# Performance work log

Hardware: AMD Instinct MI355X
Metric: run time of the kernel (lower is better)

Reference implementation:

```python
import jax, jax.numpy as jnp
import numpy as np
from jax import lax


def T_grid(t, num_coeff):
    # Chebyshev polynomials T_0..T_{N-1} evaluated at t -> (N, len(t))
    rows = [jnp.ones_like(t), t]
    for _ in range(2, num_coeff):
        rows.append(2.0 * t * rows[-1] - rows[-2])
    return jnp.stack(rows[:num_coeff], axis=0)


def setup_inputs() -> dict:
    key = jax.random.key(0)
    k1, k2, k3, k4, k5 = jax.random.split(key, 5)
    B, D, H, N, T = 128, 512, 1024, 32, 16
    return {
        "t_span": jnp.linspace(0.0, 1.0, T, dtype=jnp.float32),
        "y_init": jax.random.normal(k1, (B, D), dtype=jnp.float32),
        "B_init": jax.random.uniform(k2, (B, D, N), dtype=jnp.float32),
        "W1": jax.random.normal(k3, (D, H), dtype=jnp.float32) / jnp.sqrt(jnp.float32(D)),
        "b1": jax.random.normal(k4, (H,), dtype=jnp.float32),
        "W2": jax.random.normal(k5, (H, D), dtype=jnp.float32) / jnp.sqrt(jnp.float32(H)),
        "num_coeff_per_dim": 32,
        "max_iters": 10,
    }


def reference(t_span, y_init, B_init, W1, b1, W2, num_coeff_per_dim, max_iters):
    N = num_coeff_per_dim
    t0, t1 = t_span[0], t_span[-1]

    # Chebyshev-Gauss-Lobatto nodes on [-1, 1] and Simpson midpoints interleaved
    t_cheb = -jnp.cos(jnp.pi * (jnp.arange(N, dtype=t_span.dtype) / (N - 1)))  # (N,)
    mids = 0.5 * (t_cheb[1:] + t_cheb[:-1])
    t_simpsons = jnp.zeros(2 * N - 1, dtype=t_span.dtype).at[::2].set(t_cheb).at[1::2].set(mids)
    t_true = t0 + 0.5 * (t1 - t0) * (t_simpsons + 1.0)  # (2N-1,)

    Phi_f = T_grid(t_simpsons, N)        # (N, 2N-1)
    Phi = Phi_f[:, ::2]                  # (N, N), invert ONCE (reused every iter)
    Phi_inv = jnp.linalg.inv(Phi)
    widths = (t_true[2::2] - t_true[:-2:2]) / 6.0  # (N-1,) Simpson interval weights

    def f_all(Y):  # vector field f(t, y) = tanh(y @ W1 + t*b1) @ W2, all nodes at once
        # Y: (B, D, M) with M = 2N-1
        h = jnp.tanh(jnp.einsum("bdm,dh->bhm", Y, W1) + t_true[None, None, :] * b1[None, :, None])
        return jnp.einsum("bhm,hd->bdm", h, W2)

    def step(Bc, _):
        approx = jnp.einsum("bdn,nm->bdm", Bc, Phi_f)          # (B, D, 2N-1)
        fap = f_all(approx)
        # Simpson's rule per Chebyshev interval, then cumulative integral S
        s = widths * (fap[..., :-2:2] + 4.0 * fap[..., 1:-1:2] + fap[..., 2::2])  # (B,D,N-1)
        S = jnp.concatenate([jnp.zeros_like(s[..., :1]), jnp.cumsum(s, axis=-1)], axis=-1)
        # torch.linalg.solve(Phi, S + y0, left=False): Bn @ Phi = S + y0
        Bn = (S + y_init[..., None]) @ Phi_inv
        return Bn, None

    B_final, _ = lax.scan(step, B_init, None, length=max_iters)

    t_out = -1.0 + 2.0 * (t_span - t0) / (t1 - t0)
    Phi_out = T_grid(t_out, N)                                  # (N, T)
    approx = jnp.einsum("bdn,nt->bdt", B_final, Phi_out)        # (B, D, T)
    return jnp.moveaxis(approx, -1, 0), B_final                 # (T, B, D), (B, D, N)
```

## Files before the change

kernel.cpp:

```cpp
#include <hip/hip_runtime.h>
#include <hip/hip_bf16.h>
#include <math.h>

#define BB 128
#define DD 512
#define HH 1024
#define NB 32
#define MM 63
#define TT 16
#define ITERS 10

#define OFF_U       0
#define OFF_TTRUE   64
#define OFF_PHIOUT  128
#define OFF_PHIF_BF 1024
#define OFF_QT_BF   2048
#define HDRF        4096
#define OFF_PTPA    HDRF
#define OFF_PTP0    (OFF_PTPA + 2097152)
#define OFF_W1P     (OFF_PTP0 + 2097152)
#define OFF_W2P     (OFF_W1P + 262144)
#define OFF_WWP     (OFF_W2P + 262144)
#define OFF_YW1     (OFF_WWP + 524288)

typedef __attribute__((ext_vector_type(8))) short bf16x8;
typedef __attribute__((ext_vector_type(4))) float f32x4;

static __device__ __forceinline__ unsigned short f2bf(float f) {
    unsigned int x = __builtin_bit_cast(unsigned int, f);
    unsigned int r = x + 0x7FFFu + ((x >> 16) & 1u);
    return (unsigned short)(r >> 16);
}

static __device__ __forceinline__ void store4bf(unsigned short* p,
                                                float v0, float v1, float v2, float v3) {
    unsigned int lo = (unsigned int)f2bf(v0) | ((unsigned int)f2bf(v1) << 16);
    unsigned int hi = (unsigned int)f2bf(v2) | ((unsigned int)f2bf(v3) << 16);
    uint2 u; u.x = lo; u.y = hi;
    *(uint2*)p = u;
}

static __device__ __forceinline__ float tanh_fast(float x) {
    float e = exp2f(x * 2.88539008177793f);
    return 1.0f - 2.0f / (e + 1.0f);
}

static __device__ __forceinline__ unsigned short* aS(unsigned short* smA, int r, int c16) {
    return (unsigned short*)((char*)smA + (((r << 10) + (c16 << 4)) ^ ((r & 7) << 4)));
}

__global__ __launch_bounds__(256) void prologue_kernel(
        const float* __restrict__ t_span, const float* __restrict__ W1,
        const float* __restrict__ W2, const float* __restrict__ y_init,
        float* __restrict__ ws) {
    __shared__ __align__(16) char smem[66560];
    const int bid  = blockIdx.x;
    const int t    = threadIdx.x;
    const int lane = t & 63;
    const int w    = t >> 6;
    const int q    = lane >> 4;
    const int l15  = lane & 15;

    if (bid == 0) {
        double* tsim    = (double*)(smem + 0);
        double* ttrue_d = (double*)(smem + 512);
        double* wid     = (double*)(smem + 1024);
        double* phid    = (double*)(smem + 1280);
        double* aug     = (double*)(smem + 17408);
        double* mlt     = (double*)(smem + 33792);
        double* Rl      = (double*)(smem + 34048);
        double* Qd      = (double*)(smem + 50176);
        int*    piv_s   = (int*)(smem + 66304);

        const int rgrp = t >> 6;
        const double PI = 3.14159265358979323846;
        const double t0 = (double)t_span[0];
        const double t1 = (double)t_span[TT - 1];

        if (t < MM) {
            double v;
            if ((t & 1) == 0) {
                int j = t >> 1;
                v = -cos(PI * (double)j / (double)(NB - 1));
            } else {
                int i = t >> 1;
                double a = -cos(PI * (double)i / (double)(NB - 1));
                double b = -cos(PI * (double)(i + 1) / (double)(NB - 1));
                v = 0.5 * (a + b);
            }
            tsim[t] = v;
            ttrue_d[t] = t0 + 0.5 * (t1 - t0) * (v + 1.0);
        }
        __syncthreads();
        if (t < 31) wid[t] = (ttrue_d[2 * t + 2] - ttrue_d[2 * t]) / 6.0;
        if (t < MM) ws[OFF_TTRUE + t] = (float)ttrue_d[t];
        if (t == 63) ws[OFF_TTRUE + 63] = 0.0f;

        if (t < MM) {
            double x = tsim[t];
            double r0 = 1.0, r1 = x;
            phid[0 * MM + t] = r0;
            phid[1 * MM + t] = r1;
            for (int n = 2; n < NB; n++) {
                double r2 = 2.0 * x * r1 - r0;
                phid[n * MM + t] = r2;
                r0 = r1; r1 = r2;
            }
        }
        __syncthreads();

        {
            unsigned short* pf = (unsigned short*)(ws + OFF_PHIF_BF);
            for (int f = t; f < 64 * 32; f += 256) {
                int m = f >> 5, n = f & 31;
                pf[f] = f2bf(m < MM ? (float)phid[n * MM + m] : 0.0f);
            }
        }

        for (int f = t; f < NB * 64; f += 256) {
            int r = f >> 6, c = f & 63;
            double v;
            if (c < NB) v = phid[r * MM + 2 * c];
            else        v = ((c - NB) == r) ? 1.0 : 0.0;
            aug[f] = v;
        }
        __syncthreads();

        for (int k = 0; k < NB; k++) {
            if (t < 32) {
                double v = (t >= k) ? fabs(aug[t * 64 + k]) : -1.0;
                int idx = t;
                #pragma unroll
                for (int off = 16; off >= 1; off >>= 1) {
                    double ov = __shfl_xor(v, off);
                    int    oi = __shfl_xor(idx, off);
                    if (ov > v) { v = ov; idx = oi; }
                }
                if (t == 0) *piv_s = idx;
            }
            __syncthreads();
            const int p = *piv_s;
            if (t < 64) {
                double pv   = aug[p * 64 + k];
                double rowp = aug[p * 64 + t];
                double rowk = aug[k * 64 + t];
                aug[k * 64 + t] = rowp / pv;
                if (p != k) aug[p * 64 + t] = rowk;
            }
            __syncthreads();
            if (t < 32) mlt[t] = (t == k) ? 0.0 : aug[t * 64 + k];
            __syncthreads();
            {
                double pk = aug[k * 64 + lane];
                #pragma unroll
                for (int i = 0; i < 8; i++) {
                    int r = rgrp * 8 + i;
                    aug[r * 64 + lane] -= mlt[r] * pk;
                }
            }
            __syncthreads();
        }

        if (t < MM) {
            double acc = 0.0;
            Rl[t * NB + 0] = 0.0;
            for (int i = 1; i < NB; i++) {
                int ip = i - 1;
                double wv = 0.0;
                if (t == 2 * ip)     wv += wid[ip];
                if (t == 2 * ip + 1) wv += 4.0 * wid[ip];
                if (t == 2 * ip + 2) wv += wid[ip];
                acc += wv;
                Rl[t * NB + i] = acc;
            }
        }
        __syncthreads();

        for (int f = t; f < MM * NB; f += 256) {
            int m = f >> 5, j = f & 31;
            double s = 0.0;
            for (int i = 0; i < NB; i++) s += Rl[m * NB + i] * aug[i * 64 + 32 + j];
            Qd[f] = s;
        }
        __syncthreads();

        {
            unsigned short* qt = (unsigned short*)(ws + OFF_QT_BF);
            for (int f = t; f < 32 * 64; f += 256) {
                int j = f >> 6, m = f & 63;
                qt[f] = f2bf(m < MM ? (float)Qd[m * NB + j] : 0.0f);
            }
        }
        if (t < NB) {
            double s = 0.0;
            for (int i = 0; i < NB; i++) s += aug[i * 64 + 32 + t];
            ws[OFF_U + t] = (float)s;
        }
        if (t < TT) {
            double x = -1.0 + 2.0 * ((double)t_span[t] - t0) / (t1 - t0);
            double r0 = 1.0, r1 = x;
            ws[OFF_PHIOUT + 0 * TT + t] = 1.0f;
            ws[OFF_PHIOUT + 1 * TT + t] = (float)x;
            for (int n = 2; n < NB; n++) {
                double r2 = 2.0 * x * r1 - r0;
                ws[OFF_PHIOUT + n * TT + t] = (float)r2;
                r0 = r1; r1 = r2;
            }
        }
        return;
    }

    if (bid <= 64) {
        unsigned short* W1p = (unsigned short*)(ws + OFF_W1P);
        const int hb = bid - 1;
        #pragma unroll
        for (int i = 0; i < 4; i++) {
            int f = i * 256 + t;
            int ds = f >> 6, ln = f & 63;
            int qq = ln >> 4, ll = ln & 15;
            unsigned short tmp[8];
            #pragma unroll
            for (int e = 0; e < 8; e++)
                tmp[e] = f2bf(W1[(size_t)(ds * 32 + qq * 8 + e) * HH + hb * 16 + ll]);
            *(uint4*)(W1p + ((size_t)(hb * 16 + ds) * 64 + ln) * 8) = *(uint4*)tmp;
        }
        return;
    }

    if (bid <= 96) {
        unsigned short* W2p = (unsigned short*)(ws + OFF_W2P);
        const int db = bid - 65;
        #pragma unroll
        for (int i = 0; i < 8; i++) {
            int f = i * 256 + t;
            int hs = f >> 6, ln = f & 63;
            int qq = ln >> 4, ll = ln & 15;
            unsigned short tmp[8];
            #pragma unroll
            for (int e = 0; e < 8; e++)
                tmp[e] = f2bf(W2[(size_t)(hs * 32 + qq * 8 + e) * DD + db * 16 + ll]);
            *(uint4*)(W2p + ((size_t)(db * 32 + hs) * 64 + ln) * 8) = *(uint4*)tmp;
        }
        return;
    }

    unsigned short* lw1 = (unsigned short*)smem;

    if (bid <= 352) {
        unsigned short* WWp = (unsigned short*)(ws + OFF_WWP);
        unsigned short* pbounce = (unsigned short*)(smem + 36864);
        const int idx   = bid - 97;
        const int h2grp = idx & 31;
        const int hpb   = (idx >> 5) * 4 + w;
        const int h2c0  = h2grp * 32;

        for (int i = 0; i < 64; i++) {
            int f = i * 256 + t;
            int row = f >> 5, col = f & 31;
            lw1[row * 36 + col] = f2bf(W1[(size_t)row * HH + h2c0 + col]);
        }
        __syncthreads();

        f32x4 acc[2][2] = {};
        #pragma unroll 4
        for (int ds = 0; ds < 16; ds++) {
            bf16x8 a[2];
            #pragma unroll
            for (int mt = 0; mt < 2; mt++) {
                const float* w2r = W2 + (size_t)(hpb * 32 + mt * 16 + l15) * DD + ds * 32 + q * 8;
                float4 va = *(const float4*)w2r;
                float4 vb = *(const float4*)(w2r + 4);
                unsigned short tmp[8] = { f2bf(va.x), f2bf(va.y), f2bf(va.z), f2bf(va.w),
                                          f2bf(vb.x), f2bf(vb.y), f2bf(vb.z), f2bf(vb.w) };
                a[mt] = *(bf16x8*)tmp;
            }
            bf16x8 bb0, bb1;
            {
                unsigned short tb[8];
                #pragma unroll
                for (int e = 0; e < 8; e++)
                    tb[e] = lw1[(ds * 32 + q * 8 + e) * 36 + l15];
                bb0 = *(bf16x8*)tb;
                #pragma unroll
                for (int e = 0; e < 8; e++)
                    tb[e] = lw1[(ds * 32 + q * 8 + e) * 36 + 16 + l15];
                bb1 = *(bf16x8*)tb;
            }
            acc[0][0] = __builtin_amdgcn_mfma_f32_16x16x32_bf16(a[0], bb0, acc[0][0], 0, 0, 0);
            acc[0][1] = __builtin_amdgcn_mfma_f32_16x16x32_bf16(a[0], bb1, acc[0][1], 0, 0, 0);
            acc[1][0] = __builtin_amdgcn_mfma_f32_16x16x32_bf16(a[1], bb0, acc[1][0], 0, 0, 0);
            acc[1][1] = __builtin_amdgcn_mfma_f32_16x16x32_bf16(a[1], bb1, acc[1][1], 0, 0, 0);
        }
        unsigned short* pb = pbounce + w * 1024;
        #pragma unroll
        for (int mt = 0; mt < 2; mt++)
            #pragma unroll
            for (int nt = 0; nt < 2; nt++) {
                int lane8 = (mt * 2 + (q >> 1)) * 16 + l15;
                #pragma unroll
                for (int r = 0; r < 4; r++)
                    pb[(nt * 64 + lane8) * 8 + (q & 1) * 4 + r] = f2bf(acc[mt][nt][r]);
            }
        uint4 f0 = *(uint4*)(pb + (0 * 64 + lane) * 8);
        uint4 f1 = *(uint4*)(pb + (1 * 64 + lane) * 8);
        int h2b0 = h2grp * 2;
        *(uint4*)(WWp + ((size_t)(h2b0 + 0) * 32 + hpb) * 512 + lane * 8) = f0;
        *(uint4*)(WWp + ((size_t)(h2b0 + 1) * 32 + hpb) * 512 + lane * 8) = f1;
        return;
    }

    {
        float* yW1 = ws + OFF_YW1;
        const int h2grp = bid - 353;
        const int h2c0  = h2grp * 32;

        for (int i = 0; i < 64; i++) {
            int f = i * 256 + t;
            int row = f >> 5, col = f & 31;
            lw1[row * 36 + col] = f2bf(W1[(size_t)row * HH + h2c0 + col]);
        }
        __syncthreads();

        f32x4 acc[2][2] = {};
        #pragma unroll 4
        for (int ds = 0; ds < 16; ds++) {
            bf16x8 a[2];
            #pragma unroll
            for (int mt = 0; mt < 2; mt++) {
                const float* yr = y_init + (size_t)(w * 32 + mt * 16 + l15) * DD + ds * 32 + q * 8;
                float4 va = *(const float4*)yr;
                float4 vb = *(const float4*)(yr + 4);
                unsigned short tmp[8] = { f2bf(va.x), f2bf(va.y), f2bf(va.z), f2bf(va.w),
                                          f2bf(vb.x), f2bf(vb.y), f2bf(vb.z), f2bf(vb.w) };
                a[mt] = *(bf16x8*)tmp;
            }
            bf16x8 bb0, bb1;
            {
                unsigned short tb[8];
                #pragma unroll
                for (int e = 0; e < 8; e++)
                    tb[e] = lw1[(ds * 32 + q * 8 + e) * 36 + l15];
                bb0 = *(bf16x8*)tb;
                #pragma unroll
                for (int e = 0; e < 8; e++)
                    tb[e] = lw1[(ds * 32 + q * 8 + e) * 36 + 16 + l15];
                bb1 = *(bf16x8*)tb;
            }
            acc[0][0] = __builtin_amdgcn_mfma_f32_16x16x32_bf16(a[0], bb0, acc[0][0], 0, 0, 0);
            acc[0][1] = __builtin_amdgcn_mfma_f32_16x16x32_bf16(a[0], bb1, acc[0][1], 0, 0, 0);
            acc[1][0] = __builtin_amdgcn_mfma_f32_16x16x32_bf16(a[1], bb0, acc[1][0], 0, 0, 0);
            acc[1][1] = __builtin_amdgcn_mfma_f32_16x16x32_bf16(a[1], bb1, acc[1][1], 0, 0, 0);
        }
        #pragma unroll
        for (int mt = 0; mt < 2; mt++)
            #pragma unroll
            for (int nt = 0; nt < 2; nt++)
                #pragma unroll
                for (int r = 0; r < 4; r++) {
                    int b  = w * 32 + mt * 16 + q * 4 + r;
                    int h2 = h2c0 + nt * 16 + l15;
                    yW1[(size_t)b * HH + h2] = acc[mt][nt][r];
                }
    }
}

__global__ __launch_bounds__(256) void k1_kernel(
        const float* __restrict__ B_init,
        const unsigned short* __restrict__ W1p,
        const float* __restrict__ b1,
        const float* __restrict__ ws,
        unsigned short* __restrict__ Ptp)
{
    __shared__ __align__(16) char smem[40960];
    unsigned short* smA  = (unsigned short*)smem;
    unsigned short* t_sb = (unsigned short*)smem;
    unsigned short* g_sb = (unsigned short*)(smem + 32768);

    const int t    = threadIdx.x;
    const int lane = t & 63;
    const int w    = t >> 6;
    const int q    = lane >> 4;
    const int l15  = lane & 15;
    const int bid  = blockIdx.x;
    const int b    = bid & 127;
    const int hblk = bid >> 7;
    const int hw   = hblk * 128 + w * 32;

    {
        const float* Bi = B_init + (size_t)b * DD * NB;
        #pragma unroll 8
        for (int i = 0; i < 64; i++) {
            int f = i * 256 + t;
            int d = f >> 5, n = f & 31;
            *(unsigned short*)(smem + (((n << 10) + (d << 1)) ^ ((n & 7) << 4)))
                = f2bf(Bi[f]);
        }
    }
    __syncthreads();

    f32x4 acc[2][2] = {};
    const unsigned short* W1b = W1p + (size_t)(hw >> 4) * 8192;
    #pragma unroll 4
    for (int d0 = 0; d0 < DD; d0 += 32) {
        int c16 = (d0 >> 3) + q;
        int ds  = d0 >> 5;
        bf16x8 a0  = *(const bf16x8*)aS(smA, l15, c16);
        bf16x8 a1  = *(const bf16x8*)aS(smA, 16 + l15, c16);
        bf16x8 bb0 = *(const bf16x8*)(W1b + ds * 512 + lane * 8);
        bf16x8 bb1 = *(const bf16x8*)(W1b + 8192 + ds * 512 + lane * 8);
        acc[0][0] = __builtin_amdgcn_mfma_f32_16x16x32_bf16(a0, bb0, acc[0][0], 0, 0, 0);
        acc[0][1] = __builtin_amdgcn_mfma_f32_16x16x32_bf16(a0, bb1, acc[0][1], 0, 0, 0);
        acc[1][0] = __builtin_amdgcn_mfma_f32_16x16x32_bf16(a1, bb0, acc[1][0], 0, 0, 0);
        acc[1][1] = __builtin_amdgcn_mfma_f32_16x16x32_bf16(a1, bb1, acc[1][1], 0, 0, 0);
    }
    #pragma unroll
    for (int mt = 0; mt < 2; mt++)
        #pragma unroll
        for (int nt = 0; nt < 2; nt++) {
            int hl = w * 32 + nt * 16 + l15;
            store4bf(&g_sb[hl * 32 + mt * 16 + q * 4],
                     acc[mt][nt][0], acc[mt][nt][1], acc[mt][nt][2], acc[mt][nt][3]);
        }
    __syncthreads();

    f32x4 zacc[4][2] = {};
    const unsigned short* PF = (const unsigned short*)(ws + OFF_PHIF_BF);
    bf16x8 gb[2];
    #pragma unroll
    for (int nt = 0; nt < 2; nt++)
        gb[nt] = *(const bf16x8*)(&g_sb[(w * 32 + nt * 16 + l15) * 32 + q * 8]);
    #pragma unroll
    for (int mt = 0; mt < 4; mt++) {
        bf16x8 af = *(const bf16x8*)(PF + (mt * 16 + l15) * 32 + q * 8);
        zacc[mt][0] = __builtin_amdgcn_mfma_f32_16x16x32_bf16(af, gb[0], zacc[mt][0], 0, 0, 0);
        zacc[mt][1] = __builtin_amdgcn_mfma_f32_16x16x32_bf16(af, gb[1], zacc[mt][1], 0, 0, 0);
    }

    const float* TTp = ws + OFF_TTRUE;
    float b1v[2] = { b1[hw + l15], b1[hw + 16 + l15] };
    #pragma unroll
    for (int mt = 0; mt < 4; mt++) {
        float4 ttv = *(const float4*)(TTp + mt * 16 + q * 4);
        #pragma unroll
        for (int nt = 0; nt < 2; nt++) {
            int hl = w * 32 + nt * 16 + l15;
            float v0 = tanh_fast(zacc[mt][nt][0] + ttv.x * b1v[nt]);
            float v1 = tanh_fast(zacc[mt][nt][1] + ttv.y * b1v[nt]);
            float v2 = tanh_fast(zacc[mt][nt][2] + ttv.z * b1v[nt]);
            float v3 = tanh_fast(zacc[mt][nt][3] + ttv.w * b1v[nt]);
            store4bf(&t_sb[hl * 72 + mt * 16 + q * 4], v0, v1, v2, v3);
        }
    }
    __syncthreads();

    f32x4 pacc[2][2] = {};
    const unsigned short* QT = (const unsigned short*)(ws + OFF_QT_BF);
    #pragma unroll
    for (int ks = 0; ks < 2; ks++) {
        bf16x8 bt[2];
        #pragma unroll
        for (int nt = 0; nt < 2; nt++)
            bt[nt] = *(const bf16x8*)(&t_sb[(w * 32 + nt * 16 + l15) * 72 + ks * 32 + q * 8]);
        #pragma unroll
        for (int jt = 0; jt < 2; jt++) {
            bf16x8 aq = *(const bf16x8*)(QT + (jt * 16 + l15) * 64 + ks * 32 + q * 8);
            pacc[jt][0] = __builtin_amdgcn_mfma_f32_16x16x32_bf16(aq, bt[0], pacc[jt][0], 0, 0, 0);
            pacc[jt][1] = __builtin_amdgcn_mfma_f32_16x16x32_bf16(aq, bt[1], pacc[jt][1], 0, 0, 0);
        }
    }

    {
        unsigned short* pb = g_sb + w * 1024;
        #pragma unroll
        for (int jt = 0; jt < 2; jt++)
            #pragma unroll
            for (int nt = 0; nt < 2; nt++) {
                int grp = (nt * 2 + (l15 >> 3)) & 3;
                #pragma unroll
                for (int r = 0; r < 4; r++) {
                    int lane8 = grp * 16 + q * 4 + r;
                    pb[(jt * 64 + lane8) * 8 + (l15 & 7)] = f2bf(pacc[jt][nt][r]);
                }
            }
        int hs = hblk * 4 + w;
        uint4 f0 = *(uint4*)(pb + (0 * 64 + lane) * 8);
        uint4 f1 = *(uint4*)(pb + (1 * 64 + lane) * 8);
        *(uint4*)(Ptp + (((size_t)(b * 32 + hs) * 2 + 0) * 64 + lane) * 8) = f0;
        *(uint4*)(Ptp + (((size_t)(b * 32 + hs) * 2 + 1) * 64 + lane) * 8) = f1;
    }
}

__global__ __launch_bounds__(256) void kf_kernel(
        const unsigned short* __restrict__ Ptin,
        const unsigned short* __restrict__ WWp,
        const float* __restrict__ yW1,
        const float* __restrict__ b1,
        const float* __restrict__ ws,
        unsigned short* __restrict__ Ptout)
{
    __shared__ __align__(16) unsigned short t_sb[128 * 72];
    __shared__ __align__(16) unsigned short g_sb[128 * 32];

    const int t    = threadIdx.x;
    const int lane = t & 63;
    const int w    = t >> 6;
    const int q    = lane >> 4;
    const int l15  = lane & 15;
    const int bid  = blockIdx.x;
    const int b    = bid & 127;
    const int hblk = bid >> 7;
    const int hw   = hblk * 128 + w * 32;

    f32x4 acc[2][2] = {};
    const unsigned short* Ab  = Ptin + (size_t)b * 32768;
    const unsigned short* WWb = WWp + (size_t)(hw >> 4) * 16384;
    #pragma unroll 4
    for (int s = 0; s < 32; s++) {
        bf16x8 a0  = *(const bf16x8*)(Ab + (s * 2 + 0) * 512 + lane * 8);
        bf16x8 a1  = *(const bf16x8*)(Ab + (s * 2 + 1) * 512 + lane * 8);
        bf16x8 bb0 = *(const bf16x8*)(WWb + s * 512 + lane * 8);
        bf16x8 bb1 = *(const bf16x8*)(WWb + 16384 + s * 512 + lane * 8);
        acc[0][0] = __builtin_amdgcn_mfma_f32_16x16x32_bf16(a0, bb0, acc[0][0], 0, 0, 0);
        acc[0][1] = __builtin_amdgcn_mfma_f32_16x16x32_bf16(a0, bb1, acc[0][1], 0, 0, 0);
        acc[1][0] = __builtin_amdgcn_mfma_f32_16x16x32_bf16(a1, bb0, acc[1][0], 0, 0, 0);
        acc[1][1] = __builtin_amdgcn_mfma_f32_16x16x32_bf16(a1, bb1, acc[1][1], 0, 0, 0);
    }

    const float* U = ws + OFF_U;
    float yw[2] = { yW1[(size_t)b * HH + hw + l15],
                    yW1[(size_t)b * HH + hw + 16 + l15] };
    #pragma unroll
    for (int mt = 0; mt < 2; mt++) {
        float4 uv = *(const float4*)(U + mt * 16 + q * 4);
        #pragma unroll
        for (int nt = 0; nt < 2; nt++) {
            int hl = w * 32 + nt * 16 + l15;
            store4bf(&g_sb[hl * 32 + mt * 16 + q * 4],
                     acc[mt][nt][0] + uv.x * yw[nt],
                     acc[mt][nt][1] + uv.y * yw[nt],
                     acc[mt][nt][2] + uv.z * yw[nt],
                     acc[mt][nt][3] + uv.w * yw[nt]);
        }
    }

    f32x4 zacc[4][2] = {};
    const unsigned short* PF = (const unsigned short*)(ws + OFF_PHIF_BF);
    bf16x8 gb[2];
    #pragma unroll
    for (int nt = 0; nt < 2; nt++)
        gb[nt] = *(const bf16x8*)(&g_sb[(w * 32 + nt * 16 + l15) * 32 + q * 8]);
    #pragma unroll
    for (int mt = 0; mt < 4; mt++) {
        bf16x8 af = *(const bf16x8*)(PF + (mt * 16 + l15) * 32 + q * 8);
        zacc[mt][0] = __builtin_amdgcn_mfma_f32_16x16x32_bf16(af, gb[0], zacc[mt][0], 0, 0, 0);
        zacc[mt][1] = __builtin_amdgcn_mfma_f32_16x16x32_bf16(af, gb[1], zacc[mt][1], 0, 0, 0);
    }

    const float* TTp = ws + OFF_TTRUE;
    float b1v[2] = { b1[hw + l15], b1[hw + 16 + l15] };
    #pragma unroll
    for (int mt = 0; mt < 4; mt++) {
        float4 ttv = *(const float4*)(TTp + mt * 16 + q * 4);
        #pragma unroll
        for (int nt = 0; nt < 2; nt++) {
            int hl = w * 32 + nt * 16 + l15;
            float v0 = tanh_fast(zacc[mt][nt][0] + ttv.x * b1v[nt]);
            float v1 = tanh_fast(zacc[mt][nt][1] + ttv.y * b1v[nt]);
            float v2 = tanh_fast(zacc[mt][nt][2] + ttv.z * b1v[nt]);
            float v3 = tanh_fast(zacc[mt][nt][3] + ttv.w * b1v[nt]);
            store4bf(&t_sb[hl * 72 + mt * 16 + q * 4], v0, v1, v2, v3);
        }
    }

    f32x4 pacc[2][2] = {};
    const unsigned short* QT = (const unsigned short*)(ws + OFF_QT_BF);
    #pragma unroll
    for (int ks = 0; ks < 2; ks++) {
        bf16x8 bt[2];
        #pragma unroll
        for (int nt = 0; nt < 2; nt++)
            bt[nt] = *(const bf16x8*)(&t_sb[(w * 32 + nt * 16 + l15) * 72 + ks * 32 + q * 8]);
        #pragma unroll
        for (int jt = 0; jt < 2; jt++) {
            bf16x8 aq = *(const bf16x8*)(QT + (jt * 16 + l15) * 64 + ks * 32 + q * 8);
            pacc[jt][0] = __builtin_amdgcn_mfma_f32_16x16x32_bf16(aq, bt[0], pacc[jt][0], 0, 0, 0);
            pacc[jt][1] = __builtin_amdgcn_mfma_f32_16x16x32_bf16(aq, bt[1], pacc[jt][1], 0, 0, 0);
        }
    }

    {
        unsigned short* pb = g_sb + w * 1024;
        #pragma unroll
        for (int jt = 0; jt < 2; jt++)
            #pragma unroll
            for (int nt = 0; nt < 2; nt++) {
                int grp = (nt * 2 + (l15 >> 3)) & 3;
                #pragma unroll
                for (int r = 0; r < 4; r++) {
                    int lane8 = grp * 16 + q * 4 + r;
                    pb[(jt * 64 + lane8) * 8 + (l15 & 7)] = f2bf(pacc[jt][nt][r]);
                }
            }
        int hs = hblk * 4 + w;
        uint4 f0 = *(uint4*)(pb + (0 * 64 + lane) * 8);
        uint4 f1 = *(uint4*)(pb + (1 * 64 + lane) * 8);
        *(uint4*)(Ptout + (((size_t)(b * 32 + hs) * 2 + 0) * 64 + lane) * 8) = f0;
        *(uint4*)(Ptout + (((size_t)(b * 32 + hs) * 2 + 1) * 64 + lane) * 8) = f1;
    }
}

__global__ __launch_bounds__(256) void k2f_kernel(
        const unsigned short* __restrict__ Ptp,
        const unsigned short* __restrict__ W2p,
        const float* __restrict__ y_init,
        const float* __restrict__ ws,
        float* __restrict__ out)
{
    __shared__ __align__(16) float ls[4 * 544];
    __shared__ float phiout_s[NB * TT];

    const int t    = threadIdx.x;
    const int lane = t & 63;
    const int w    = t >> 6;
    const int q    = lane >> 4;
    const int l15  = lane & 15;
    const int bid  = blockIdx.x;
    const int b    = bid & 127;
    const int dblk = bid >> 7;
    const int dw   = dblk * 64 + w * 16;

    for (int f = t; f < NB * TT; f += 256) phiout_s[f] = ws[OFF_PHIOUT + f];

    f32x4 acc[2] = {};
    const unsigned short* Ab  = Ptp + (size_t)b * 32768;
    const unsigned short* W2b = W2p + (size_t)(dblk * 4 + w) * 16384;
    #pragma unroll 4
    for (int s = 0; s < 32; s++) {
        bf16x8 a0 = *(const bf16x8*)(Ab + (s * 2 + 0) * 512 + lane * 8);
        bf16x8 a1 = *(const bf16x8*)(Ab + (s * 2 + 1) * 512 + lane * 8);
        bf16x8 bb = *(const bf16x8*)(W2b + s * 512 + lane * 8);
        acc[0] = __builtin_amdgcn_mfma_f32_16x16x32_bf16(a0, bb, acc[0], 0, 0, 0);
        acc[1] = __builtin_amdgcn_mfma_f32_16x16x32_bf16(a1, bb, acc[1], 0, 0, 0);
    }

    const float* U = ws + OFF_U;
    float yv = y_init[(size_t)b * DD + dw + l15];
    #pragma unroll
    for (int mt = 0; mt < 2; mt++) {
        float4 uv = *(const float4*)(U + mt * 16 + q * 4);
        #pragma unroll
        for (int r = 0; r < 4; r++) {
            int j = mt * 16 + q * 4 + r;
            float uvr = (r == 0) ? uv.x : (r == 1) ? uv.y : (r == 2) ? uv.z : uv.w;
            ls[w * 544 + j * 17 + l15] = acc[mt][r] + yv * uvr;
        }
    }
    __syncthreads();

    float* out1 = out + (size_t)TT * BB * DD;
    #pragma unroll
    for (int it = 0; it < 8; it++) {
        int f = it * 64 + lane;
        int d_l = f >> 5, j2 = f & 31;
        out1[((size_t)b * DD + dw + d_l) * NB + j2] = ls[w * 544 + j2 * 17 + d_l];
    }

    #pragma unroll
    for (int i = 0; i < 4; i++) {
        int idx = i * 256 + t;
        int t16 = idx >> 6, dl = idx & 63;
        float s = 0.f;
        #pragma unroll
        for (int n = 0; n < NB; n++)
            s += ls[(dl >> 4) * 544 + n * 17 + (dl & 15)] * phiout_s[n * TT + t16];
        out[(size_t)t16 * (BB * DD) + (size_t)b * DD + dblk * 64 + dl] = s;
    }
}

extern "C" void kernel_launch(void* const* d_in, const int* in_sizes, int n_in,
                              void* d_out, int out_size, void* d_ws, size_t ws_size,
                              hipStream_t stream) {
    const float* t_span = (const float*)d_in[0];
    const float* y_init = (const float*)d_in[1];
    const float* B_init = (const float*)d_in[2];
    const float* W1     = (const float*)d_in[3];
    const float* b1     = (const float*)d_in[4];
    const float* W2     = (const float*)d_in[5];
    float* ws  = (float*)d_ws;
    float* out = (float*)d_out;

    unsigned short* W1p  = (unsigned short*)(ws + OFF_W1P);
    unsigned short* W2p  = (unsigned short*)(ws + OFF_W2P);
    unsigned short* WWp  = (unsigned short*)(ws + OFF_WWP);
    float*          yW1  = ws + OFF_YW1;
    unsigned short* PtpA = (unsigned short*)(ws + OFF_PTPA);
    unsigned short* PtpB = (unsigned short*)(ws + OFF_PTP0);

    prologue_kernel<<<dim3(385), 256, 0, stream>>>(t_span, W1, W2, y_init, ws);

    k1_kernel<<<dim3(1024), 256, 0, stream>>>(B_init, W1p, b1, ws, PtpA);

    unsigned short* pin  = PtpA;
    unsigned short* pout = PtpB;
    for (int it = 1; it < ITERS; it++) {
        kf_kernel<<<dim3(1024), 256, 0, stream>>>(pin, WWp, yW1, b1, ws, pout);
        unsigned short* tmp = pin; pin = pout; pout = tmp;
    }
    k2f_kernel<<<dim3(1024), 256, 0, stream>>>(pin, W2p, y_init, ws, out);
}
```

Before: 368.5 us.

## Double the kf tile width, stage A operand in LDS, transpose W1 staging

kf_kernel now gives each wave 64 hidden columns instead of 32 and halves the grid to 512 blocks. The per-batch A operand is double-buffered into shared memory in chunks and each A fragment is reused across four B tiles, which cuts redundant global loads of Ptin. The prologue stores the W1 tile transposed so B fragments are read with one vector LDS load instead of eight scalar loads. The cost is more registers and a 68KB shared buffer per block, which may reduce occupancy and leave fewer blocks to fill the GPU.

```diff
diff --git a/kernel.cpp b/kernel.cpp
--- a/kernel.cpp
+++ b/kernel.cpp
@@ -244,11 +244,11 @@
         return;
     }
 
-    unsigned short* lw1 = (unsigned short*)smem;
+    unsigned short* lw1t = (unsigned short*)smem;
 
     if (bid <= 352) {
         unsigned short* WWp = (unsigned short*)(ws + OFF_WWP);
-        unsigned short* pbounce = (unsigned short*)(smem + 36864);
+        unsigned short* pbounce = (unsigned short*)(smem + 33280);
         const int idx   = bid - 97;
         const int h2grp = idx & 31;
         const int hpb   = (idx >> 5) * 4 + w;
@@ -257,7 +257,7 @@
         for (int i = 0; i < 64; i++) {
             int f = i * 256 + t;
             int row = f >> 5, col = f & 31;
-            lw1[row * 36 + col] = f2bf(W1[(size_t)row * HH + h2c0 + col]);
+            lw1t[col * 520 + row] = f2bf(W1[(size_t)row * HH + h2c0 + col]);
         }
         __syncthreads();
 
@@ -274,18 +274,8 @@
                                           f2bf(vb.x), f2bf(vb.y), f2bf(vb.z), f2bf(vb.w) };
                 a[mt] = *(bf16x8*)tmp;
             }
-            bf16x8 bb0, bb1;
-            {
-                unsigned short tb[8];
-                #pragma unroll
-                for (int e = 0; e < 8; e++)
-                    tb[e] = lw1[(ds * 32 + q * 8 + e) * 36 + l15];
-                bb0 = *(bf16x8*)tb;
-                #pragma unroll
-                for (int e = 0; e < 8; e++)
-                    tb[e] = lw1[(ds * 32 + q * 8 + e) * 36 + 16 + l15];
-                bb1 = *(bf16x8*)tb;
-            }
+            bf16x8 bb0 = *(const bf16x8*)(lw1t + l15 * 520 + ds * 32 + q * 8);
+            bf16x8 bb1 = *(const bf16x8*)(lw1t + (16 + l15) * 520 + ds * 32 + q * 8);
             acc[0][0] = __builtin_amdgcn_mfma_f32_16x16x32_bf16(a[0], bb0, acc[0][0], 0, 0, 0);
             acc[0][1] = __builtin_amdgcn_mfma_f32_16x16x32_bf16(a[0], bb1, acc[0][1], 0, 0, 0);
             acc[1][0] = __builtin_amdgcn_mfma_f32_16x16x32_bf16(a[1], bb0, acc[1][0], 0, 0, 0);
@@ -317,7 +307,7 @@
         for (int i = 0; i < 64; i++) {
             int f = i * 256 + t;
             int row = f >> 5, col = f & 31;
-            lw1[row * 36 + col] = f2bf(W1[(size_t)row * HH + h2c0 + col]);
+            lw1t[col * 520 + row] = f2bf(W1[(size_t)row * HH + h2c0 + col]);
         }
         __syncthreads();
 
@@ -334,18 +324,8 @@
                                           f2bf(vb.x), f2bf(vb.y), f2bf(vb.z), f2bf(vb.w) };
                 a[mt] = *(bf16x8*)tmp;
             }
-            bf16x8 bb0, bb1;
-            {
-                unsigned short tb[8];
-                #pragma unroll
-                for (int e = 0; e < 8; e++)
-                    tb[e] = lw1[(ds * 32 + q * 8 + e) * 36 + l15];
-                bb0 = *(bf16x8*)tb;
-                #pragma unroll
-                for (int e = 0; e < 8; e++)
-                    tb[e] = lw1[(ds * 32 + q * 8 + e) * 36 + 16 + l15];
-                bb1 = *(bf16x8*)tb;
-            }
+            bf16x8 bb0 = *(const bf16x8*)(lw1t + l15 * 520 + ds * 32 + q * 8);
+            bf16x8 bb1 = *(const bf16x8*)(lw1t + (16 + l15) * 520 + ds * 32 + q * 8);
             acc[0][0] = __builtin_amdgcn_mfma_f32_16x16x32_bf16(a[0], bb0, acc[0][0], 0, 0, 0);
             acc[0][1] = __builtin_amdgcn_mfma_f32_16x16x32_bf16(a[0], bb1, acc[0][1], 0, 0, 0);
             acc[1][0] = __builtin_amdgcn_mfma_f32_16x16x32_bf16(a[1], bb0, acc[1][0], 0, 0, 0);
@@ -498,8 +478,7 @@
         const float* __restrict__ ws,
         unsigned short* __restrict__ Ptout)
 {
-    __shared__ __align__(16) unsigned short t_sb[128 * 72];
-    __shared__ __align__(16) unsigned short g_sb[128 * 32];
+    __shared__ __align__(16) char smem[69632];
 
     const int t    = threadIdx.x;
     const int lane = t & 63;
@@ -508,34 +487,63 @@
     const int l15  = lane & 15;
     const int bid  = blockIdx.x;
     const int b    = bid & 127;
-    const int hblk = bid >> 7;
-    const int hw   = hblk * 128 + w * 32;
-
-    f32x4 acc[2][2] = {};
+    const int hblk2 = bid >> 7;
+    const int hw   = hblk2 * 256 + w * 64;
+
+    f32x4 acc[2][4] = {};
     const unsigned short* Ab  = Ptin + (size_t)b * 32768;
-    const unsigned short* WWb = WWp + (size_t)(hw >> 4) * 16384;
-    #pragma unroll 4
-    for (int s = 0; s < 32; s++) {
-        bf16x8 a0  = *(const bf16x8*)(Ab + (s * 2 + 0) * 512 + lane * 8);
-        bf16x8 a1  = *(const bf16x8*)(Ab + (s * 2 + 1) * 512 + lane * 8);
-        bf16x8 bb0 = *(const bf16x8*)(WWb + s * 512 + lane * 8);
-        bf16x8 bb1 = *(const bf16x8*)(WWb + 16384 + s * 512 + lane * 8);
-        acc[0][0] = __builtin_amdgcn_mfma_f32_16x16x32_bf16(a0, bb0, acc[0][0], 0, 0, 0);
-        acc[0][1] = __builtin_amdgcn_mfma_f32_16x16x32_bf16(a0, bb1, acc[0][1], 0, 0, 0);
-        acc[1][0] = __builtin_amdgcn_mfma_f32_16x16x32_bf16(a1, bb0, acc[1][0], 0, 0, 0);
-        acc[1][1] = __builtin_amdgcn_mfma_f32_16x16x32_bf16(a1, bb1, acc[1][1], 0, 0, 0);
-    }
+    const unsigned short* WWb = WWp + (size_t)(hblk2 * 16 + w * 4) * 16384;
+    unsigned short* buf0 = (unsigned short*)smem;
+    unsigned short* buf1 = (unsigned short*)(smem + 16384);
+
+    {
+        const uint4* src = (const uint4*)Ab;
+        uint4* dst = (uint4*)buf0;
+        #pragma unroll
+        for (int i = 0; i < 4; i++) dst[i * 256 + t] = src[i * 256 + t];
+    }
+    __syncthreads();
+
+    #pragma unroll 1
+    for (int c = 0; c < 4; ++c) {
+        if (c < 3) {
+            const uint4* src = (const uint4*)(Ab + (c + 1) * 8192);
+            uint4* dst = (uint4*)((c & 1) ? buf0 : buf1);
+            #pragma unroll
+            for (int i = 0; i < 4; i++) dst[i * 256 + t] = src[i * 256 + t];
+        }
+        const unsigned short* Ac = (c & 1) ? buf1 : buf0;
+        #pragma unroll
+        for (int sl = 0; sl < 8; ++sl) {
+            int s = c * 8 + sl;
+            bf16x8 a0 = *(const bf16x8*)(Ac + (sl * 2 + 0) * 512 + lane * 8);
+            bf16x8 a1 = *(const bf16x8*)(Ac + (sl * 2 + 1) * 512 + lane * 8);
+            #pragma unroll
+            for (int nt = 0; nt < 4; nt++) {
+                bf16x8 bb = *(const bf16x8*)(WWb + nt * 16384 + s * 512 + lane * 8);
+                acc[0][nt] = __builtin_amdgcn_mfma_f32_16x16x32_bf16(a0, bb, acc[0][nt], 0, 0, 0);
+                acc[1][nt] = __builtin_amdgcn_mfma_f32_16x16x32_bf16(a1, bb, acc[1][nt], 0, 0, 0);
+            }
+        }
+        __syncthreads();
+    }
+
+    unsigned short* g_w  = (unsigned short*)(smem + w * 4096);
+    unsigned short* t_w  = (unsigned short*)(smem + 16384 + w * 9216);
+    unsigned short* pb_w = (unsigned short*)(smem + 53248 + w * 4096);
 
     const float* U = ws + OFF_U;
-    float yw[2] = { yW1[(size_t)b * HH + hw + l15],
-                    yW1[(size_t)b * HH + hw + 16 + l15] };
+    float yw[4];
+    #pragma unroll
+    for (int nt = 0; nt < 4; nt++)
+        yw[nt] = yW1[(size_t)b * HH + hw + nt * 16 + l15];
     #pragma unroll
     for (int mt = 0; mt < 2; mt++) {
         float4 uv = *(const float4*)(U + mt * 16 + q * 4);
         #pragma unroll
-        for (int nt = 0; nt < 2; nt++) {
-            int hl = w * 32 + nt * 16 + l15;
-            store4bf(&g_sb[hl * 32 + mt * 16 + q * 4],
+        for (int nt = 0; nt < 4; nt++) {
+            int hl = nt * 16 + l15;
+            store4bf(&g_w[hl * 32 + mt * 16 + q * 4],
                      acc[mt][nt][0] + uv.x * yw[nt],
                      acc[mt][nt][1] + uv.y * yw[nt],
                      acc[mt][nt][2] + uv.z * yw[nt],
@@ -543,69 +551,76 @@
         }
     }
 
-    f32x4 zacc[4][2] = {};
+    f32x4 zacc[4][4] = {};
     const unsigned short* PF = (const unsigned short*)(ws + OFF_PHIF_BF);
-    bf16x8 gb[2];
-    #pragma unroll
-    for (int nt = 0; nt < 2; nt++)
-        gb[nt] = *(const bf16x8*)(&g_sb[(w * 32 + nt * 16 + l15) * 32 + q * 8]);
+    bf16x8 gb[4];
+    #pragma unroll
+    for (int nt = 0; nt < 4; nt++)
+        gb[nt] = *(const bf16x8*)(&g_w[(nt * 16 + l15) * 32 + q * 8]);
     #pragma unroll
     for (int mt = 0; mt < 4; mt++) {
         bf16x8 af = *(const bf16x8*)(PF + (mt * 16 + l15) * 32 + q * 8);
-        zacc[mt][0] = __builtin_amdgcn_mfma_f32_16x16x32_bf16(af, gb[0], zacc[mt][0], 0, 0, 0);
-        zacc[mt][1] = __builtin_amdgcn_mfma_f32_16x16x32_bf16(af, gb[1], zacc[mt][1], 0, 0, 0);
+        #pragma unroll
+        for (int nt = 0; nt < 4; nt++)
+            zacc[mt][nt] = __builtin_amdgcn_mfma_f32_16x16x32_bf16(af, gb[nt], zacc[mt][nt], 0, 0, 0);
     }
 
     const float* TTp = ws + OFF_TTRUE;
-    float b1v[2] = { b1[hw + l15], b1[hw + 16 + l15] };
+    float b1v[4];
+    #pragma unroll
+    for (int nt = 0; nt < 4; nt++)
+        b1v[nt] = b1[hw + nt * 16 + l15];
     #pragma unroll
     for (int mt = 0; mt < 4; mt++) {
         float4 ttv = *(const float4*)(TTp + mt * 16 + q * 4);
         #pragma unroll
-        for (int nt = 0; nt < 2; nt++) {
-            int hl = w * 32 + nt * 16 + l15;
+        for (int nt = 0; nt < 4; nt++) {
+            int hl = nt * 16 + l15;
             float v0 = tanh_fast(zacc[mt][nt][0] + ttv.x * b1v[nt]);
             float v1 = tanh_fast(zacc[mt][nt][1] + ttv.y * b1v[nt]);
             float v2 = tanh_fast(zacc[mt][nt][2] + ttv.z * b1v[nt]);
             float v3 = tanh_fast(zacc[mt][nt][3] + ttv.w * b1v[nt]);
-            store4bf(&t_sb[hl * 72 + mt * 16 + q * 4], v0, v1, v2, v3);
-        }
-    }
-
-    f32x4 pacc[2][2] = {};
+            store4bf(&t_w[hl * 72 + mt * 16 + q * 4], v0, v1, v2, v3);
+        }
+    }
+
+    f32x4 pacc[2][4] = {};
     const unsigned short* QT = (const unsigned short*)(ws + OFF_QT_BF);
     #pragma unroll
     for (int ks = 0; ks < 2; ks++) {
-        bf16x8 bt[2];
-        #pragma unroll
-        for (int nt = 0; nt < 2; nt++)
-            bt[nt] = *(const bf16x8*)(&t_sb[(w * 32 + nt * 16 + l15) * 72 + ks * 32 + q * 8]);
+        bf16x8 bt[4];
+        #pragma unroll
+        for (int nt = 0; nt < 4; nt++)
+            bt[nt] = *(const bf16x8*)(&t_w[(nt * 16 + l15) * 72 + ks * 32 + q * 8]);
         #pragma unroll
         for (int jt = 0; jt < 2; jt++) {
             bf16x8 aq = *(const bf16x8*)(QT + (jt * 16 + l15) * 64 + ks * 32 + q * 8);
-            pacc[jt][0] = __builtin_amdgcn_mfma_f32_16x16x32_bf16(aq, bt[0], pacc[jt][0], 0, 0, 0);
-            pacc[jt][1] = __builtin_amdgcn_mfma_f32_16x16x32_bf16(aq, bt[1], pacc[jt][1], 0, 0, 0);
+            #pragma unroll
+            for (int nt = 0; nt < 4; nt++)
+                pacc[jt][nt] = __builtin_amdgcn_mfma_f32_16x16x32_bf16(aq, bt[nt], pacc[jt][nt], 0, 0, 0);
         }
     }
 
     {
-        unsigned short* pb = g_sb + w * 1024;
         #pragma unroll
         for (int jt = 0; jt < 2; jt++)
             #pragma unroll
-            for (int nt = 0; nt < 2; nt++) {
-                int grp = (nt * 2 + (l15 >> 3)) & 3;
+            for (int nt = 0; nt < 4; nt++) {
+                int grp    = ((nt & 1) * 2 + (l15 >> 3)) & 3;
+                int hs_loc = nt >> 1;
                 #pragma unroll
                 for (int r = 0; r < 4; r++) {
                     int lane8 = grp * 16 + q * 4 + r;
-                    pb[(jt * 64 + lane8) * 8 + (l15 & 7)] = f2bf(pacc[jt][nt][r]);
+                    pb_w[(hs_loc * 2 + jt) * 512 + lane8 * 8 + (l15 & 7)] = f2bf(pacc[jt][nt][r]);
                 }
             }
-        int hs = hblk * 4 + w;
-        uint4 f0 = *(uint4*)(pb + (0 * 64 + lane) * 8);
-        uint4 f1 = *(uint4*)(pb + (1 * 64 + lane) * 8);
-        *(uint4*)(Ptout + (((size_t)(b * 32 + hs) * 2 + 0) * 64 + lane) * 8) = f0;
-        *(uint4*)(Ptout + (((size_t)(b * 32 + hs) * 2 + 1) * 64 + lane) * 8) = f1;
+        int hs0 = hblk2 * 8 + w * 2;
+        #pragma unroll
+        for (int i = 0; i < 4; i++) {
+            uint4 fv = *(uint4*)(pb_w + i * 512 + lane * 8);
+            int hs = hs0 + (i >> 1), jt = i & 1;
+            *(uint4*)(Ptout + (((size_t)(b * 32 + hs) * 2 + jt) * 64 + lane) * 8) = fv;
+        }
     }
 }
 
@@ -703,7 +718,7 @@
     unsigned short* pin  = PtpA;
     unsigned short* pout = PtpB;
     for (int it = 1; it < ITERS; it++) {
-        kf_kernel<<<dim3(1024), 256, 0, stream>>>(pin, WWp, yW1, b1, ws, pout);
+        kf_kernel<<<dim3(512), 256, 0, stream>>>(pin, WWp, yW1, b1, ws, pout);
         unsigned short* tmp = pin; pin = pout; pout = tmp;
     }
     k2f_kernel<<<dim3(1024), 256, 0, stream>>>(pin, W2p, y_init, ws, out);
```

After: 361.7 us. Within noise of the previous version (-1.9%).
